# Kernel optimization log

Measured on AMD Instinct MI355X. Metric: run time of the kernel, lower is better.

## Reference

```python
import jax, jax.numpy as jnp
import numpy as np

KERNEL = 7
STRIDE = 3
C_IN, C_OUT = 3, 4
HIDDEN, OUTPUT = 64, 10
H_OUT = (32 - KERNEL) // STRIDE + 1  # 9
FC1_IN = C_OUT * H_OUT * H_OUT       # 324


def setup_inputs() -> dict:
    key = jax.random.key(0)
    ks = jax.random.split(key, 6)
    B = 16384
    x = jax.random.normal(ks[0], (B, C_IN, 32, 32), dtype=jnp.float32)
    conv_w = jax.random.normal(ks[1], (C_OUT, C_IN, KERNEL, KERNEL), dtype=jnp.float32) * 0.05
    fc1_w = jax.random.normal(ks[2], (HIDDEN, FC1_IN), dtype=jnp.float32) * (1.0 / np.sqrt(FC1_IN))
    fc1_b = jax.random.normal(ks[3], (HIDDEN,), dtype=jnp.float32) * 0.01
    fc2_w = jax.random.normal(ks[4], (OUTPUT, HIDDEN), dtype=jnp.float32) * (1.0 / np.sqrt(HIDDEN))
    fc2_b = jax.random.normal(ks[5], (OUTPUT,), dtype=jnp.float32) * 0.01
    return {"x": x, "conv_w": conv_w, "fc1_w": fc1_w, "fc1_b": fc1_b, "fc2_w": fc2_w, "fc2_b": fc2_b}


def reference(x, conv_w, fc1_w, fc1_b, fc2_w, fc2_b):
    # conv (NO bias, matching original forward which only uses conv1.weight)
    y = jax.lax.conv_general_dilated(
        x, conv_w, window_strides=(STRIDE, STRIDE), padding='VALID',
        dimension_numbers=('NCHW', 'OIHW', 'NCHW'))  # [B, 4, 9, 9]
    y = y * y
    y = y.reshape(y.shape[0], -1)                    # [B, 324]
    h = y @ fc1_w.T + fc1_b                          # [B, 64]
    h = h * h
    out = h @ fc2_w.T + fc2_b                        # [B, 10]
    return out
```

## Files before the change

### kernel.cpp

```cpp
#include <hip/hip_runtime.h>
#include <string.h>


typedef _Float16 f16;
typedef f16 f16x8 __attribute__((ext_vector_type(8)));
typedef __fp16 fp16x2 __attribute__((ext_vector_type(2)));
typedef float f32x4 __attribute__((ext_vector_type(4)));
typedef unsigned long long ull;

#define YSQ_B   27648
#define LDS_B   (27648 + 11520)
#define BUFB    13824

__device__ __forceinline__ unsigned pack_rtz(float a, float b) {
    fp16x2 h = __builtin_amdgcn_cvt_pkrtz(a, b);
    unsigned u; memcpy(&u, &h, 4); return u;
}

__device__ __forceinline__ void stage_pair(f16* XSH, int buf, const float4 ld[6], int t) {
#pragma unroll
    for (int i = 0; i < 6; ++i) {
        int idx = i * 256 + t;
        int sp  = idx >= 768;
        int within = idx - sp * 768;
        int ci  = within >> 8;
        int rem = within & 255;
        int row = rem >> 3;
        int q   = rem & 7;
        int h0  = buf * 6912 + sp * 3456 + ci * 1152 + row * 36 + q * 4;
        float4 v = ld[i];
        unsigned u0 = pack_rtz(v.x, v.y), u1 = pack_rtz(v.z, v.w);
        *(ull*)(XSH + h0) = ((ull)u1 << 32) | u0;
    }
}

__global__ void prep_weights(const float* __restrict__ cw, const float* __restrict__ fc1w,
                             f16* __restrict__ w1t, f16* __restrict__ wct) {
    int idx = blockIdx.x * 256 + threadIdx.x;
    if (idx < 45056) {
        int part = idx / 22528;
        int rem  = idx % 22528;
        int n = rem / 352, k = rem % 352;
        float v = (k < 324) ? fc1w[n * 324 + k] : 0.f;
        f16 hi = (f16)v;
        w1t[idx] = (part == 0) ? hi : (f16)(v - (float)hi);
    } else if (idx < 45056 + 6144) {
        int j = idx - 45056;
        int part = j / 3072;
        int rem  = j % 3072;
        int oc = rem / 192, k = rem % 192;
        int seg = k >> 3, kw = k & 7;
        float v = 0.f;
        if (oc < 4 && seg < 21 && kw < 7) {
            int ci = seg / 7, kh = seg % 7;
            v = cw[((oc * 3 + ci) * 7 + kh) * 7 + kw];
        }
        f16 hi = (f16)v;
        wct[j] = (part == 0) ? hi : (f16)(v - (float)hi);
    }
}

__global__ __launch_bounds__(256, 4) void convnet_mfma(
    const float* __restrict__ x,
    const f16*  __restrict__ w1t,
    const f16*  __restrict__ wct,
    const float* __restrict__ fc1b,
    const float* __restrict__ fc2w,
    const float* __restrict__ fc2b,
    float* __restrict__ out)
{
    __shared__ unsigned char lds[LDS_B];
    f16* XSH = (f16*)lds;
    f16* YS = (f16*)(lds + YSQ_B);
    float* HSQ = (float*)lds;

    const int t    = threadIdx.x;
    const int lane = t & 63;
    const int w    = t >> 6;
    const int g    = lane >> 4;
    const int lr   = lane & 15;
    const size_t base_s = (size_t)blockIdx.x * 16;

    f16x8 wc[2][6];
#pragma unroll
    for (int part = 0; part < 2; ++part)
#pragma unroll
        for (int st = 0; st < 6; ++st)
            wc[part][st] = *(const f16x8*)(wct + part * 3072 + lr * 192 + st * 32 + g * 8);

    int segoff[6];
#pragma unroll
    for (int st = 0; st < 6; ++st) {
        int seg  = st * 4 + g;
        int segc = seg > 20 ? 20 : seg;
        int ci   = segc >= 14 ? 2 : (segc >= 7 ? 1 : 0);
        int kh   = segc - ci * 7;
        segoff[st] = 2304 * ci + 72 * kh;
    }
    const int ntiles = (w == 3) ? 2 : 3;
    int bA[3], shv[3], coff[3][4];
#pragma unroll
    for (int ti = 0; ti < 3; ++ti) {
        int tile = w + ti * 4;
        int grow = tile * 16 + lr;
        int growc = grow > 161 ? 161 : grow;
        int sp  = growc >= 81;
        int p   = growc - (sp ? 81 : 0);
        int oh  = (p * 57) >> 9;
        int ow  = p - oh * 9;
        int c3  = 3 * ow;
        int resid = c3 & 3;
        bA[ti]  = sp * 6912 + 216 * oh + 8 * (c3 >> 2) + ((resid >= 2) ? 4 : 0);
        shv[ti] = (resid & 1) << 4;
#pragma unroll
        for (int r = 0; r < 4; ++r) {
            int gr = tile * 16 + g * 4 + r;
            if (ti < ntiles && gr < 162) {
                int sp2 = gr >= 81;
                int p2  = gr - (sp2 ? 81 : 0);
                coff[ti][r] = sp2 * 360 + lr * 81 + p2;
            } else coff[ti][r] = -1;
        }
    }

    float4 ld[6];
    {
        const float4* xg = (const float4*)(x + base_s * 3072);
#pragma unroll
        for (int i = 0; i < 6; ++i) ld[i] = xg[i * 256 + t];
    }
#pragma unroll
    for (int i = 0; i < 3; ++i) {
        int idx = i * 256 + t;
        if (idx < 720) *(f32x4*)(lds + YSQ_B + idx * 16) = f32x4{0.f, 0.f, 0.f, 0.f};
    }
    stage_pair(XSH, 0, ld, t);
    __syncthreads();

    int bufB = 0;
    for (int pair = 0; pair < 8; ++pair) {
        if (pair < 7) {
            const float4* xg = (const float4*)(x + (base_s + (size_t)(pair + 1) * 2) * 3072);
#pragma unroll
            for (int i = 0; i < 6; ++i) ld[i] = xg[i * 256 + t];
        }
        f16* ysp = YS + pair * 720;
#pragma unroll
        for (int ti = 0; ti < 3; ++ti) {
            if (ti < ntiles) {
                const unsigned char* pA = lds + (bufB + bA[ti]);
                const int sh = shv[ti];
                f32x4 acc = {0.f, 0.f, 0.f, 0.f};
#pragma unroll
                for (int st = 0; st < 6; ++st) {
                    const unsigned* q = (const unsigned*)(pA + segoff[st]);
                    unsigned r0 = q[0], r1 = q[1], r2 = q[2], r3 = q[3];
                    union { unsigned u[4]; f16x8 h; } af;
                    af.u[0] = __builtin_amdgcn_alignbit(r1, r0, sh);
                    af.u[1] = __builtin_amdgcn_alignbit(r2, r1, sh);
                    af.u[2] = __builtin_amdgcn_alignbit(r3, r2, sh);
                    af.u[3] = __builtin_amdgcn_alignbit(r3, r3, sh);
                    acc = __builtin_amdgcn_mfma_f32_16x16x32_f16(af.h, wc[0][st], acc, 0, 0, 0);
                    acc = __builtin_amdgcn_mfma_f32_16x16x32_f16(af.h, wc[1][st], acc, 0, 0, 0);
                }
                if (lr < 4) {
#pragma unroll
                    for (int r = 0; r < 4; ++r) {
                        int off = coff[ti][r];
                        if (off >= 0) {
                            float y = acc[r];
                            ysp[off] = (f16)(y * y);
                        }
                    }
                }
            }
        }
        if (pair < 7) stage_pair(XSH, bufB ? 0 : 1, ld, t);
        __syncthreads();
        bufB ^= BUFB;
    }

    {
        f32x4 a1 = {0.f, 0.f, 0.f, 0.f};
        const int n = w * 16 + lr;
#pragma unroll
        for (int st = 0; st < 11; ++st) {
            f16x8 av = *(const f16x8*)(YS + lr * 360 + st * 32 + g * 8);
            f16x8 bh = *(const f16x8*)(w1t +          n * 352 + st * 32 + g * 8);
            f16x8 bl = *(const f16x8*)(w1t + 22528 +  n * 352 + st * 32 + g * 8);
            a1 = __builtin_amdgcn_mfma_f32_16x16x32_f16(av, bh, a1, 0, 0, 0);
            a1 = __builtin_amdgcn_mfma_f32_16x16x32_f16(av, bl, a1, 0, 0, 0);
        }
        float bias = fc1b[n];
#pragma unroll
        for (int r = 0; r < 4; ++r) {
            int s = g * 4 + r;
            float h = a1[r] + bias;
            HSQ[s * 65 + n] = h * h;
        }
    }
    __syncthreads();

    if (t < 160) {
        int sj = t / 10, j = t - sj * 10;
        float a = fc2b[j];
        const float* wr = fc2w + j * 64;
        const float* hv = &HSQ[sj * 65];
#pragma unroll
        for (int i = 0; i < 64; ++i) a += wr[i] * hv[i];
        out[(base_s + sj) * 10 + j] = a;
    }
}

extern "C" void kernel_launch(void* const* d_in, const int* in_sizes, int n_in,
                              void* d_out, int out_size, void* d_ws, size_t ws_size,
                              hipStream_t stream) {
    const float* x    = (const float*)d_in[0];
    const float* cw   = (const float*)d_in[1];
    const float* fc1w = (const float*)d_in[2];
    const float* fc1b = (const float*)d_in[3];
    const float* fc2w = (const float*)d_in[4];
    const float* fc2b = (const float*)d_in[5];
    float* out = (float*)d_out;

    f16* w1t = (f16*)d_ws;
    f16* wct = w1t + 45056;

    hipLaunchKernelGGL(prep_weights, dim3(200), dim3(256), 0, stream, cw, fc1w, w1t, wct);

    const int B = in_sizes[0] / 3072;
    hipLaunchKernelGGL(convnet_mfma, dim3(B / 16), dim3(256), 0, stream,
                       x, w1t, wct, fc1b, fc2w, fc2b, out);
}
```

Baseline: 50.62 us.

## Stage pre-shifted im2col windows in LDS and drop conv lo-weight MFMA

Staging now writes each input row as pre-aligned 8-element windows per output column, so the conv A-operand becomes one 16-byte LDS load instead of four 32-bit loads plus alignbit shifts. The conv MFMA pass that used the low-order fp16 split of the weights is dropped, halving conv MFMA work but losing that extra weight precision. Double buffering is removed: only 192 threads load 8 float4 each, and an extra barrier per pair separates compute from the restaging write. The tile assignment across waves also changes.

```diff
diff --git a/kernel.cpp b/kernel.cpp
--- a/kernel.cpp
+++ b/kernel.cpp
@@ -6,31 +6,37 @@
 typedef f16 f16x8 __attribute__((ext_vector_type(8)));
 typedef __fp16 fp16x2 __attribute__((ext_vector_type(2)));
 typedef float f32x4 __attribute__((ext_vector_type(4)));
-typedef unsigned long long ull;
-
-#define YSQ_B   27648
-#define LDS_B   (27648 + 11520)
-#define BUFB    13824
+
+#define YS_B   27648
+#define LDS_B  (27648 + 11520)
 
 __device__ __forceinline__ unsigned pack_rtz(float a, float b) {
     fp16x2 h = __builtin_amdgcn_cvt_pkrtz(a, b);
     unsigned u; memcpy(&u, &h, 4); return u;
 }
 
-__device__ __forceinline__ void stage_pair(f16* XSH, int buf, const float4 ld[6], int t) {
-#pragma unroll
-    for (int i = 0; i < 6; ++i) {
-        int idx = i * 256 + t;
-        int sp  = idx >= 768;
-        int within = idx - sp * 768;
-        int ci  = within >> 8;
-        int rem = within & 255;
-        int row = rem >> 3;
-        int q   = rem & 7;
-        int h0  = buf * 6912 + sp * 3456 + ci * 1152 + row * 36 + q * 4;
-        float4 v = ld[i];
-        unsigned u0 = pack_rtz(v.x, v.y), u1 = pack_rtz(v.z, v.w);
-        *(ull*)(XSH + h0) = ((ull)u1 << 32) | u0;
+__device__ __forceinline__ void write_windows(f16* wptr, const float4 ldv[8]) {
+    unsigned h[16];
+#pragma unroll
+    for (int i = 0; i < 8; ++i) {
+        h[2*i]   = pack_rtz(ldv[i].x, ldv[i].y);
+        h[2*i+1] = pack_rtz(ldv[i].z, ldv[i].w);
+    }
+#pragma unroll
+    for (int ow = 0; ow < 9; ow += 2) {
+        int d = (3 * ow) >> 1;
+        uint4 v; v.x = h[d]; v.y = h[d+1]; v.z = h[d+2]; v.w = h[d+3];
+        *reinterpret_cast<uint4*>(wptr + ow * 8) = v;
+    }
+#pragma unroll
+    for (int ow = 1; ow < 9; ow += 2) {
+        int d = (3 * ow) >> 1;
+        uint4 v;
+        v.x = __builtin_amdgcn_alignbit(h[d+1], h[d],   16);
+        v.y = __builtin_amdgcn_alignbit(h[d+2], h[d+1], 16);
+        v.z = __builtin_amdgcn_alignbit(h[d+3], h[d+2], 16);
+        v.w = __builtin_amdgcn_alignbit(h[d+4], h[d+3], 16);
+        *reinterpret_cast<uint4*>(wptr + ow * 8) = v;
     }
 }
 
@@ -70,8 +76,8 @@
     float* __restrict__ out)
 {
     __shared__ unsigned char lds[LDS_B];
-    f16* XSH = (f16*)lds;
-    f16* YS = (f16*)(lds + YSQ_B);
+    f16* WINH = (f16*)lds;
+    f16* YS   = (f16*)(lds + YS_B);
     float* HSQ = (float*)lds;
 
     const int t    = threadIdx.x;
@@ -81,37 +87,33 @@
     const int lr   = lane & 15;
     const size_t base_s = (size_t)blockIdx.x * 16;
 
-    f16x8 wc[2][6];
-#pragma unroll
-    for (int part = 0; part < 2; ++part)
-#pragma unroll
-        for (int st = 0; st < 6; ++st)
-            wc[part][st] = *(const f16x8*)(wct + part * 3072 + lr * 192 + st * 32 + g * 8);
-
-    int segoff[6];
+    f16x8 wcf[6];
+#pragma unroll
+    for (int st = 0; st < 6; ++st)
+        wcf[st] = *(const f16x8*)(wct + lr * 192 + st * 32 + g * 8);
+
+    int seg2off[6];
 #pragma unroll
     for (int st = 0; st < 6; ++st) {
         int seg  = st * 4 + g;
         int segc = seg > 20 ? 20 : seg;
         int ci   = segc >= 14 ? 2 : (segc >= 7 ? 1 : 0);
         int kh   = segc - ci * 7;
-        segoff[st] = 2304 * ci + 72 * kh;
-    }
-    const int ntiles = (w == 3) ? 2 : 3;
-    int bA[3], shv[3], coff[3][4];
+        seg2off[st] = ci * 4608 + kh * 144;
+    }
+    const int ntiles = (w == 2) ? 2 : 3;
+    int rowbase[3], coff[3][4];
 #pragma unroll
     for (int ti = 0; ti < 3; ++ti) {
         int tile = w + ti * 4;
+        if (w == 3 && ti == 2) tile = 10;
         int grow = tile * 16 + lr;
         int growc = grow > 161 ? 161 : grow;
         int sp  = growc >= 81;
         int p   = growc - (sp ? 81 : 0);
         int oh  = (p * 57) >> 9;
         int ow  = p - oh * 9;
-        int c3  = 3 * ow;
-        int resid = c3 & 3;
-        bA[ti]  = sp * 6912 + 216 * oh + 8 * (c3 >> 2) + ((resid >= 2) ? 4 : 0);
-        shv[ti] = (resid & 1) << 4;
+        rowbase[ti] = sp * 13824 + oh * 432 + ow * 16;
 #pragma unroll
         for (int r = 0; r < 4; ++r) {
             int gr = tile * 16 + g * 4 + r;
@@ -123,45 +125,44 @@
         }
     }
 
-    float4 ld[6];
-    {
-        const float4* xg = (const float4*)(x + base_s * 3072);
-#pragma unroll
-        for (int i = 0; i < 6; ++i) ld[i] = xg[i * 256 + t];
+    const bool stg = t < 192;
+    const int ssp  = (t >= 96) ? 1 : 0;
+    const int srem = t - ssp * 96;
+    const int sci  = srem >> 5;
+    const int srow = srem & 31;
+    const int goff = sci * 1024 + srow * 32;
+    f16* wptr = WINH + ssp * 6912 + sci * 2304 + srow * 72;
+
+    float4 ldv[8];
+    if (stg) {
+        const float* gp = x + (base_s + ssp) * 3072 + goff;
+#pragma unroll
+        for (int i = 0; i < 8; ++i) ldv[i] = *(const float4*)(gp + 4 * i);
     }
 #pragma unroll
     for (int i = 0; i < 3; ++i) {
         int idx = i * 256 + t;
-        if (idx < 720) *(f32x4*)(lds + YSQ_B + idx * 16) = f32x4{0.f, 0.f, 0.f, 0.f};
-    }
-    stage_pair(XSH, 0, ld, t);
+        if (idx < 720) *(f32x4*)(lds + YS_B + idx * 16) = f32x4{0.f, 0.f, 0.f, 0.f};
+    }
+    if (stg) write_windows(wptr, ldv);
     __syncthreads();
 
-    int bufB = 0;
     for (int pair = 0; pair < 8; ++pair) {
-        if (pair < 7) {
-            const float4* xg = (const float4*)(x + (base_s + (size_t)(pair + 1) * 2) * 3072);
-#pragma unroll
-            for (int i = 0; i < 6; ++i) ld[i] = xg[i * 256 + t];
+        if (pair < 7 && stg) {
+            const float* gp = x + (base_s + (size_t)(pair + 1) * 2 + ssp) * 3072 + goff;
+#pragma unroll
+            for (int i = 0; i < 8; ++i) ldv[i] = *(const float4*)(gp + 4 * i);
         }
         f16* ysp = YS + pair * 720;
 #pragma unroll
         for (int ti = 0; ti < 3; ++ti) {
             if (ti < ntiles) {
-                const unsigned char* pA = lds + (bufB + bA[ti]);
-                const int sh = shv[ti];
+                const unsigned char* pA = lds + rowbase[ti];
                 f32x4 acc = {0.f, 0.f, 0.f, 0.f};
 #pragma unroll
                 for (int st = 0; st < 6; ++st) {
-                    const unsigned* q = (const unsigned*)(pA + segoff[st]);
-                    unsigned r0 = q[0], r1 = q[1], r2 = q[2], r3 = q[3];
-                    union { unsigned u[4]; f16x8 h; } af;
-                    af.u[0] = __builtin_amdgcn_alignbit(r1, r0, sh);
-                    af.u[1] = __builtin_amdgcn_alignbit(r2, r1, sh);
-                    af.u[2] = __builtin_amdgcn_alignbit(r3, r2, sh);
-                    af.u[3] = __builtin_amdgcn_alignbit(r3, r3, sh);
-                    acc = __builtin_amdgcn_mfma_f32_16x16x32_f16(af.h, wc[0][st], acc, 0, 0, 0);
-                    acc = __builtin_amdgcn_mfma_f32_16x16x32_f16(af.h, wc[1][st], acc, 0, 0, 0);
+                    f16x8 af = *(const f16x8*)(pA + seg2off[st]);
+                    acc = __builtin_amdgcn_mfma_f32_16x16x32_f16(af, wcf[st], acc, 0, 0, 0);
                 }
                 if (lr < 4) {
 #pragma unroll
@@ -175,9 +176,11 @@
                 }
             }
         }
-        if (pair < 7) stage_pair(XSH, bufB ? 0 : 1, ld, t);
         __syncthreads();
-        bufB ^= BUFB;
+        if (pair < 7) {
+            if (stg) write_windows(wptr, ldv);
+            __syncthreads();
+        }
     }
 
     {
```

Result: slower. 52.25 us (+3.2%).
